# Kernel tuning notes

Measured on AMD Instinct MI355X. Metric: run time of the kernel, lower is better.

The kernel has to match this reference:

```python
import jax, jax.numpy as jnp
import numpy as np

C = 1.0          # ball curvature (manifold.c)
EPS = 1e-15      # norm clamp
BALL_EPS = 1e-5  # projection margin


def _norm(x):
    # clamped L2 norm over last dim, kept dim
    return jnp.clip(jnp.linalg.norm(x, axis=-1, keepdims=True), EPS, None)


def _artanh(x):
    return jnp.arctanh(jnp.clip(x, -1.0 + 1e-7, 1.0 - 1e-7))


def _proj(x, c):
    # project onto the Poincare ball of radius (1-eps)/sqrt(c)
    norm = _norm(x)
    maxnorm = (1.0 - BALL_EPS) / jnp.sqrt(c)
    return jnp.where(norm > maxnorm, x / norm * maxnorm, x)


def _expmap0(u, c):
    sc = jnp.sqrt(c)
    n = _norm(u)
    return jnp.tanh(sc * n) * u / (sc * n)


def _mobius_matvec(W, x, c):
    # tanh(||Mx||/||x|| * artanh(sqrt(c)||x||)) * Mx / (sqrt(c)||Mx||)
    sc = jnp.sqrt(c)
    mx = x @ W.T                      # [N, d_out]
    xn = _norm(x)
    mxn = _norm(mx)
    return jnp.tanh(mxn / xn * _artanh(sc * xn)) * mx / (mxn * sc)


def _mobius_add(x, y, c):
    x2 = jnp.sum(x * x, axis=-1, keepdims=True)
    y2 = jnp.sum(y * y, axis=-1, keepdims=True)
    xy = jnp.sum(x * y, axis=-1, keepdims=True)
    num = (1.0 + 2.0 * c * xy + c * y2) * x + (1.0 - c * x2) * y
    den = 1.0 + 2.0 * c * xy + c * c * x2 * y2
    return num / jnp.clip(den, EPS, None)


def setup_inputs() -> dict:
    key = jax.random.key(0)
    k1, k2, k3 = jax.random.split(key, 3)
    N, d_in, d_out = 2097152, 64, 64
    # points must lie inside the unit ball: small gaussian then projection
    x = _proj(0.01 * jax.random.normal(k1, (N, d_in), jnp.float32), C)
    # xavier_uniform with gain sqrt(2)
    bound = np.sqrt(2.0) * np.sqrt(6.0 / (d_in + d_out))
    weight = jax.random.uniform(k2, (d_out, d_in), jnp.float32, -bound, bound)
    bias = 0.01 * jax.random.normal(k3, (d_out,), jnp.float32)
    return {"x": x, "weight": weight, "bias": bias}


def reference(x, weight, bias):
    # activation=None, p_drop=0 path of CustomHyperbolicLinear.forward
    mv = _mobius_matvec(weight, x, C)
    res = _proj(mv, C)
    bias_tan = bias.reshape(1, -1)               # proj_tan0 is identity on the ball
    hyp_bias = _proj(_expmap0(bias_tan, C), C)   # [1, d_out]
    res = _mobius_add(res, hyp_bias, C)
    res = _proj(res, C)
    return res
```

## Files before the change

### kernel.cpp

```cpp
#include <hip/hip_runtime.h>
#include <hip/hip_bf16.h>


typedef __bf16 bf16x8 __attribute__((ext_vector_type(8)));
typedef float  f32x4  __attribute__((ext_vector_type(4)));

#define MAXN 0.99999f
#define EPSN 1e-15f

__global__ __launch_bounds__(256)
void hyp_lin_kernel(const float* __restrict__ X, const float* __restrict__ W,
                    const float* __restrict__ Bv, float* __restrict__ O, int nrows)
{
    const int lane = threadIdx.x & 63;
    const int lg = lane >> 4;
    const int lm = lane & 15;
    const int gwave = blockIdx.x * 4 + (threadIdx.x >> 6);
    const int nwaves = gridDim.x * 4;

    bf16x8 bfrag[4][2];
#pragma unroll
    for (int t = 0; t < 4; ++t) {
        const float* wrow = W + (t * 16 + lm) * 64;
#pragma unroll
        for (int c = 0; c < 2; ++c) {
            const float4 w0 = *reinterpret_cast<const float4*>(wrow + c * 32 + lg * 8);
            const float4 w1 = *reinterpret_cast<const float4*>(wrow + c * 32 + lg * 8 + 4);
            bf16x8 f;
            f[0] = (__bf16)w0.x; f[1] = (__bf16)w0.y; f[2] = (__bf16)w0.z; f[3] = (__bf16)w0.w;
            f[4] = (__bf16)w1.x; f[5] = (__bf16)w1.y; f[6] = (__bf16)w1.z; f[7] = (__bf16)w1.w;
            bfrag[t][c] = f;
        }
    }

    float braw[4];
    float bn2 = 0.f;
#pragma unroll
    for (int t = 0; t < 4; ++t) { braw[t] = Bv[t * 16 + lm]; bn2 += braw[t] * braw[t]; }
#pragma unroll
    for (int m = 1; m <= 8; m <<= 1) bn2 += __shfl_xor(bn2, m);
    const float bn = fmaxf(sqrtf(bn2), EPSN);
    const float tb = tanhf(bn);
    float bscale = tb / bn;
    if (fabsf(tb) > MAXN) bscale *= MAXN / fabsf(tb);
    float hb[4];
#pragma unroll
    for (int t = 0; t < 4; ++t) hb[t] = braw[t] * bscale;
    const float y2 = bscale * bscale * bn2;

    const int ntiles = (nrows + 15) >> 4;
    for (int tile = gwave; tile < ntiles; tile += nwaves) {
        const int rb = tile << 4;
        int lrow = rb + lm; if (lrow > nrows - 1) lrow = nrows - 1;
        const float* xp = X + (size_t)lrow * 64 + lg * 8;
        const float4 x0 = *reinterpret_cast<const float4*>(xp);
        const float4 x1 = *reinterpret_cast<const float4*>(xp + 4);
        const float4 x2 = *reinterpret_cast<const float4*>(xp + 32);
        const float4 x3 = *reinterpret_cast<const float4*>(xp + 36);

        float xs = x0.x*x0.x + x0.y*x0.y + x0.z*x0.z + x0.w*x0.w
                 + x1.x*x1.x + x1.y*x1.y + x1.z*x1.z + x1.w*x1.w
                 + x2.x*x2.x + x2.y*x2.y + x2.z*x2.z + x2.w*x2.w
                 + x3.x*x3.x + x3.y*x3.y + x3.z*x3.z + x3.w*x3.w;
        xs += __shfl_xor(xs, 16);
        xs += __shfl_xor(xs, 32);

        bf16x8 a0, a1;
        a0[0]=(__bf16)x0.x; a0[1]=(__bf16)x0.y; a0[2]=(__bf16)x0.z; a0[3]=(__bf16)x0.w;
        a0[4]=(__bf16)x1.x; a0[5]=(__bf16)x1.y; a0[6]=(__bf16)x1.z; a0[7]=(__bf16)x1.w;
        a1[0]=(__bf16)x2.x; a1[1]=(__bf16)x2.y; a1[2]=(__bf16)x2.z; a1[3]=(__bf16)x2.w;
        a1[4]=(__bf16)x3.x; a1[5]=(__bf16)x3.y; a1[6]=(__bf16)x3.z; a1[7]=(__bf16)x3.w;

        f32x4 acc[4];
#pragma unroll
        for (int t = 0; t < 4; ++t) {
            f32x4 z = {0.f, 0.f, 0.f, 0.f};
            z = __builtin_amdgcn_mfma_f32_16x16x32_bf16(a0, bfrag[t][0], z, 0, 0, 0);
            z = __builtin_amdgcn_mfma_f32_16x16x32_bf16(a1, bfrag[t][1], z, 0, 0, 0);
            acc[t] = z;
        }

        float m2[4] = {0,0,0,0}, dd[4] = {0,0,0,0};
#pragma unroll
        for (int t = 0; t < 4; ++t)
#pragma unroll
            for (int r = 0; r < 4; ++r) {
                const float v = acc[t][r];
                m2[r] += v * v;
                dd[r] += v * hb[t];
            }
#pragma unroll
        for (int r = 0; r < 4; ++r)
#pragma unroll
            for (int m = 1; m <= 8; m <<= 1) {
                m2[r] += __shfl_xor(m2[r], m);
                dd[r] += __shfl_xor(dd[r], m);
            }

        float aa[4], gg[4];
#pragma unroll
        for (int r = 0; r < 4; ++r) {
            const float xn2 = __shfl(xs, 4 * lg + r);
            const float xn  = fmaxf(sqrtf(xn2), EPSN);
            const float mxn = fmaxf(sqrtf(m2[r]), EPSN);
            const float xc  = fminf(xn, 1.f - 1e-7f);
            const float at  = 0.5f * log1pf(2.f * xc / (1.f - xc));
            const float th  = tanhf((mxn / xn) * at);
            float s = th / mxn;
            if (th > MAXN) s *= MAXN / th;
            const float x2v = s * s * m2[r];
            const float xy  = s * dd[r];
            const float A_  = 1.f + 2.f * xy + y2;
            const float B_  = 1.f - x2v;
            float den = 1.f + 2.f * xy + x2v * y2;
            den = fmaxf(den, EPSN);
            float a_ = A_ * s / den;
            float g_ = B_ / den;
            const float nn2 = a_ * a_ * m2[r] + 2.f * a_ * g_ * dd[r] + g_ * g_ * y2;
            const float nn  = sqrtf(nn2);
            if (nn > MAXN) { const float sc = MAXN / nn; a_ *= sc; g_ *= sc; }
            aa[r] = a_; gg[r] = g_;
        }

#pragma unroll
        for (int r = 0; r < 4; ++r) {
            const int orow = rb + 4 * lg + r;
            if (orow < nrows) {
                float* op = O + (size_t)orow * 64 + lm;
#pragma unroll
                for (int t = 0; t < 4; ++t)
                    op[t * 16] = aa[r] * acc[t][r] + gg[r] * hb[t];
            }
        }
    }
}

extern "C" void kernel_launch(void* const* d_in, const int* in_sizes, int n_in,
                              void* d_out, int out_size, void* d_ws, size_t ws_size,
                              hipStream_t stream)
{
    const float* X = (const float*)d_in[0];
    const float* W = (const float*)d_in[1];
    const float* B = (const float*)d_in[2];
    float* O = (float*)d_out;
    const int nrows = in_sizes[0] / 64;
    hipLaunchKernelGGL(hyp_lin_kernel, dim3(2048), dim3(256), 0, stream, X, W, B, O, nrows);
}
```

Before: 898.8 us.

## Swap MFMA operands so each lane owns one row and stores float4

Swaps the MFMA operand roles so W is the A operand and X is the B operand. Each lane's accumulator then holds four consecutive output columns of a single row instead of one column across four rows. This lets each lane store float4 vectors rather than scattered scalar writes. It also cuts the per-row reductions to two cross-lane shuffles and runs the scalar hyperbolic math once per lane instead of four times. The bias is now loaded per lane in the matching column layout.

```diff
diff --git a/kernel.cpp b/kernel.cpp
--- a/kernel.cpp
+++ b/kernel.cpp
@@ -18,7 +18,7 @@
     const int gwave = blockIdx.x * 4 + (threadIdx.x >> 6);
     const int nwaves = gridDim.x * 4;
 
-    bf16x8 bfrag[4][2];
+    bf16x8 wfrag[4][2];
 #pragma unroll
     for (int t = 0; t < 4; ++t) {
         const float* wrow = W + (t * 16 + lm) * 64;
@@ -29,23 +29,30 @@
             bf16x8 f;
             f[0] = (__bf16)w0.x; f[1] = (__bf16)w0.y; f[2] = (__bf16)w0.z; f[3] = (__bf16)w0.w;
             f[4] = (__bf16)w1.x; f[5] = (__bf16)w1.y; f[6] = (__bf16)w1.z; f[7] = (__bf16)w1.w;
-            bfrag[t][c] = f;
+            wfrag[t][c] = f;
         }
     }
 
-    float braw[4];
+    float hb[4][4];
     float bn2 = 0.f;
 #pragma unroll
-    for (int t = 0; t < 4; ++t) { braw[t] = Bv[t * 16 + lm]; bn2 += braw[t] * braw[t]; }
+    for (int t = 0; t < 4; ++t)
 #pragma unroll
-    for (int m = 1; m <= 8; m <<= 1) bn2 += __shfl_xor(bn2, m);
+        for (int r = 0; r < 4; ++r) {
+            const float b = Bv[t * 16 + lg * 4 + r];
+            hb[t][r] = b;
+            bn2 += b * b;
+        }
+    bn2 += __shfl_xor(bn2, 16);
+    bn2 += __shfl_xor(bn2, 32);
     const float bn = fmaxf(sqrtf(bn2), EPSN);
     const float tb = tanhf(bn);
     float bscale = tb / bn;
     if (fabsf(tb) > MAXN) bscale *= MAXN / fabsf(tb);
-    float hb[4];
 #pragma unroll
-    for (int t = 0; t < 4; ++t) hb[t] = braw[t] * bscale;
+    for (int t = 0; t < 4; ++t)
+#pragma unroll
+        for (int r = 0; r < 4; ++r) hb[t][r] *= bscale;
     const float y2 = bscale * bscale * bn2;
 
     const int ntiles = (nrows + 15) >> 4;
@@ -65,71 +72,62 @@
         xs += __shfl_xor(xs, 16);
         xs += __shfl_xor(xs, 32);
 
-        bf16x8 a0, a1;
-        a0[0]=(__bf16)x0.x; a0[1]=(__bf16)x0.y; a0[2]=(__bf16)x0.z; a0[3]=(__bf16)x0.w;
-        a0[4]=(__bf16)x1.x; a0[5]=(__bf16)x1.y; a0[6]=(__bf16)x1.z; a0[7]=(__bf16)x1.w;
-        a1[0]=(__bf16)x2.x; a1[1]=(__bf16)x2.y; a1[2]=(__bf16)x2.z; a1[3]=(__bf16)x2.w;
-        a1[4]=(__bf16)x3.x; a1[5]=(__bf16)x3.y; a1[6]=(__bf16)x3.z; a1[7]=(__bf16)x3.w;
+        bf16x8 b0, b1;
+        b0[0]=(__bf16)x0.x; b0[1]=(__bf16)x0.y; b0[2]=(__bf16)x0.z; b0[3]=(__bf16)x0.w;
+        b0[4]=(__bf16)x1.x; b0[5]=(__bf16)x1.y; b0[6]=(__bf16)x1.z; b0[7]=(__bf16)x1.w;
+        b1[0]=(__bf16)x2.x; b1[1]=(__bf16)x2.y; b1[2]=(__bf16)x2.z; b1[3]=(__bf16)x2.w;
+        b1[4]=(__bf16)x3.x; b1[5]=(__bf16)x3.y; b1[6]=(__bf16)x3.z; b1[7]=(__bf16)x3.w;
 
         f32x4 acc[4];
 #pragma unroll
         for (int t = 0; t < 4; ++t) {
             f32x4 z = {0.f, 0.f, 0.f, 0.f};
-            z = __builtin_amdgcn_mfma_f32_16x16x32_bf16(a0, bfrag[t][0], z, 0, 0, 0);
-            z = __builtin_amdgcn_mfma_f32_16x16x32_bf16(a1, bfrag[t][1], z, 0, 0, 0);
+            z = __builtin_amdgcn_mfma_f32_16x16x32_bf16(wfrag[t][0], b0, z, 0, 0, 0);
+            z = __builtin_amdgcn_mfma_f32_16x16x32_bf16(wfrag[t][1], b1, z, 0, 0, 0);
             acc[t] = z;
         }
 
-        float m2[4] = {0,0,0,0}, dd[4] = {0,0,0,0};
+        float m2 = 0.f, dd = 0.f;
 #pragma unroll
         for (int t = 0; t < 4; ++t)
 #pragma unroll
             for (int r = 0; r < 4; ++r) {
                 const float v = acc[t][r];
-                m2[r] += v * v;
-                dd[r] += v * hb[t];
+                m2 += v * v;
+                dd += v * hb[t][r];
             }
+        m2 += __shfl_xor(m2, 16);  m2 += __shfl_xor(m2, 32);
+        dd += __shfl_xor(dd, 16);  dd += __shfl_xor(dd, 32);
+
+        const float xn  = fmaxf(sqrtf(xs), EPSN);
+        const float mxn = fmaxf(sqrtf(m2), EPSN);
+        const float xc  = fminf(xn, 1.f - 1e-7f);
+        const float at  = 0.5f * log1pf(2.f * xc / (1.f - xc));
+        const float th  = tanhf((mxn / xn) * at);
+        float s = th / mxn;
+        if (th > MAXN) s *= MAXN / th;
+        const float x2v = s * s * m2;
+        const float xy  = s * dd;
+        const float A_  = 1.f + 2.f * xy + y2;
+        const float B_  = 1.f - x2v;
+        float den = 1.f + 2.f * xy + x2v * y2;
+        den = fmaxf(den, EPSN);
+        float a_ = A_ * s / den;
+        float g_ = B_ / den;
+        const float nn2 = a_ * a_ * m2 + 2.f * a_ * g_ * dd + g_ * g_ * y2;
+        const float nn  = sqrtf(nn2);
+        if (nn > MAXN) { const float sc = MAXN / nn; a_ *= sc; g_ *= sc; }
+
+        if (rb + lm < nrows) {
+            float* op = O + (size_t)(rb + lm) * 64 + lg * 4;
 #pragma unroll
-        for (int r = 0; r < 4; ++r)
-#pragma unroll
-            for (int m = 1; m <= 8; m <<= 1) {
-                m2[r] += __shfl_xor(m2[r], m);
-                dd[r] += __shfl_xor(dd[r], m);
-            }
-
-        float aa[4], gg[4];
-#pragma unroll
-        for (int r = 0; r < 4; ++r) {
-            const float xn2 = __shfl(xs, 4 * lg + r);
-            const float xn  = fmaxf(sqrtf(xn2), EPSN);
-            const float mxn = fmaxf(sqrtf(m2[r]), EPSN);
-            const float xc  = fminf(xn, 1.f - 1e-7f);
-            const float at  = 0.5f * log1pf(2.f * xc / (1.f - xc));
-            const float th  = tanhf((mxn / xn) * at);
-            float s = th / mxn;
-            if (th > MAXN) s *= MAXN / th;
-            const float x2v = s * s * m2[r];
-            const float xy  = s * dd[r];
-            const float A_  = 1.f + 2.f * xy + y2;
-            const float B_  = 1.f - x2v;
-            float den = 1.f + 2.f * xy + x2v * y2;
-            den = fmaxf(den, EPSN);
-            float a_ = A_ * s / den;
-            float g_ = B_ / den;
-            const float nn2 = a_ * a_ * m2[r] + 2.f * a_ * g_ * dd[r] + g_ * g_ * y2;
-            const float nn  = sqrtf(nn2);
-            if (nn > MAXN) { const float sc = MAXN / nn; a_ *= sc; g_ *= sc; }
-            aa[r] = a_; gg[r] = g_;
-        }
-
-#pragma unroll
-        for (int r = 0; r < 4; ++r) {
-            const int orow = rb + 4 * lg + r;
-            if (orow < nrows) {
-                float* op = O + (size_t)orow * 64 + lm;
-#pragma unroll
-                for (int t = 0; t < 4; ++t)
-                    op[t * 16] = aa[r] * acc[t][r] + gg[r] * hb[t];
+            for (int t = 0; t < 4; ++t) {
+                float4 o;
+                o.x = a_ * acc[t][0] + g_ * hb[t][0];
+                o.y = a_ * acc[t][1] + g_ * hb[t][1];
+                o.z = a_ * acc[t][2] + g_ * hb[t][2];
+                o.w = a_ * acc[t][3] + g_ * hb[t][3];
+                *reinterpret_cast<float4*>(op + t * 16) = o;
             }
         }
     }
```

Measured after the change: 854.4 us. -4.9%, faster.
